# Performance work log

Measured on AMD Instinct MI355X. Metric: run time of the kernel, lower is better.

The kernel has to match this reference:

```python
import jax, jax.numpy as jnp
import numpy as np

NUM_CLASSES = 10
PGD_NUMS = 10
ALPHA = 0.15
# Hardcoded in the original module: sign vector for 10 classes
SIGN_VEC = jnp.array([-1.0] * 4 + [1.0] * 6, dtype=jnp.float32)


def setup_inputs() -> dict:
    key = jax.random.key(0)
    k1, k2, k3 = jax.random.split(key, 3)
    B = 1048576
    logit = jax.random.normal(k1, (B, NUM_CLASSES), dtype=jnp.float32)
    y = jax.random.randint(k2, (B,), 0, NUM_CLASSES, dtype=jnp.int32)
    label_freq = jax.random.randint(k3, (NUM_CLASSES,), 0, PGD_NUMS, dtype=jnp.int32)
    return {"logit": logit, "y": y, "label_freq": label_freq}


def _compute_adv(logit, y):
    # softmax over classes, then per-class mean of softmax rows (one-hot^T @ p)
    p = jax.nn.softmax(logit, axis=-1)  # [B, C]
    sum_class_logit = jax.ops.segment_sum(p, y, num_segments=NUM_CLASSES)  # [C, C]
    counts = jax.ops.segment_sum(jnp.ones(y.shape[0], dtype=logit.dtype), y,
                                 num_segments=NUM_CLASSES)  # [C]
    counts = jnp.where(counts == 0, jnp.asarray(100.0, logit.dtype), counts)
    mean_class_logit = sum_class_logit / counts[:, None]  # [C, C]
    grad = mean_class_logit - jnp.eye(NUM_CLASSES, dtype=logit.dtype)
    # Faithful to torch: norm over dim=0 (columns), then reshape(-1,1) divides row i
    col_norm = jnp.linalg.norm(grad, axis=0)  # [C]
    grad = grad / col_norm[:, None]
    grad = ALPHA * grad * SIGN_VEC[:, None].astype(logit.dtype)
    return grad[y]  # index_select along dim 0 -> [B, C]


def reference(logit, y, label_freq):
    logit_copy = logit

    def step(l, _):
        l_new = l + _compute_adv(l, y)
        return l_new, l_new

    _, logit_steps = jax.lax.scan(step, logit, None, length=PGD_NUMS)  # [P, B, C]

    # Original: logit_news = sum_i logit_steps[label_freq[i]] * (y == i)
    # Since class masks are disjoint, this is a per-sample gather of step label_freq[y[n]].
    steps_per_sample = label_freq[y]  # [B]
    B = logit.shape[0]
    logit_news = logit_steps[steps_per_sample, jnp.arange(B)]  # [B, C]

    # mean cross-entropy
    log_p = jax.nn.log_softmax(logit_news, axis=-1)
    loss_adv = -jnp.mean(jnp.take_along_axis(log_p, y[:, None].astype(jnp.int32), axis=1))
    return loss_adv, logit_news, logit_copy
```

## Files before the change

### kernel.cpp

```cpp
#include <hip/hip_runtime.h>

#define NC 10
#define PGD 10
#define ALPHA 0.15f
#define NTAB 32

#define WS_COUNTS 0
#define WS_STAB   320
#define WS_DGLOB  32320
#define WS_ZERO_N 32320

__device__ __forceinline__ void table_from_stats(
    const float* __restrict__ S_tab_t,
    const float* __restrict__ counts_tab,
    const float* __restrict__ Dprev,
    float* sh_D, float* sh_tmp, float* sh_cnt, float* sh_cn, int tid)
{
    if (tid < 10) {
        float s = 0.f;
        for (int k = 0; k < NTAB; ++k) s += counts_tab[k * 10 + tid];
        sh_cnt[tid] = (s == 0.f) ? 100.f : s;
    }
    if (tid < 100) {
        float s = 0.f;
        for (int k = 0; k < NTAB; ++k) s += S_tab_t[k * 100 + tid];
        sh_tmp[tid] = s;
    }
    __syncthreads();
    if (tid < 100) {
        int c = tid / 10, j = tid - c * 10;
        float g = sh_tmp[tid] / sh_cnt[c] - ((c == j) ? 1.f : 0.f);
        sh_tmp[tid] = g;
    }
    __syncthreads();
    if (tid < 10) {
        float s = 0.f;
        for (int cc = 0; cc < 10; ++cc) { float g = sh_tmp[cc * 10 + tid]; s += g * g; }
        sh_cn[tid] = sqrtf(s);
    }
    __syncthreads();
    if (tid < 100) {
        int c = tid / 10;
        float sign = (c < 4) ? -1.f : 1.f;
        float g = sh_tmp[tid] / sh_cn[c] * (ALPHA * sign);
        sh_D[tid] = (Dprev ? Dprev[tid] : 0.f) + g;
    }
    __syncthreads();
}

__global__ void k_init(float* __restrict__ ws, float* __restrict__ out) {
    int i = blockIdx.x * blockDim.x + threadIdx.x;
    if (i == 0) out[0] = 0.f;
    int gs = gridDim.x * blockDim.x;
    for (int k = i; k < WS_ZERO_N; k += gs) ws[k] = 0.f;
}

__global__ __launch_bounds__(256) void k_step(
    const float* __restrict__ logit, const int* __restrict__ y,
    float* __restrict__ ws, int B, int t , int spt)
{
    __shared__ float sh_D[100];
    __shared__ float sh_tmp[100];
    __shared__ float sh_cnt[10];
    __shared__ float sh_cn[10];
    __shared__ float wtab[4][100];
    __shared__ float ctab[4][10];
    const int tid = threadIdx.x;

    float* counts_tab = ws + WS_COUNTS;
    float* S_tab      = ws + WS_STAB;
    float* D_glob     = ws + WS_DGLOB;

    if (t >= 2) {
        const float* Dprev = (t == 2) ? nullptr : (D_glob + (size_t)(t - 3) * 100);
        table_from_stats(S_tab + (size_t)(t - 2) * (NTAB * 100), counts_tab, Dprev,
                         sh_D, sh_tmp, sh_cnt, sh_cn, tid);
        if (blockIdx.x == 0 && tid < 100) D_glob[(size_t)(t - 2) * 100 + tid] = sh_D[tid];
    }
    for (int i = tid; i < 400; i += 256) (&wtab[0][0])[i] = 0.f;
    if (t == 1) for (int i = tid; i < 40; i += 256) (&ctab[0][0])[i] = 0.f;
    __syncthreads();

    const int w = tid >> 6;
    const int gthreads = gridDim.x * blockDim.x;
    const int base = blockIdx.x * blockDim.x + tid;
    for (int k = 0; k < spt; ++k) {
        int idx = base + k * gthreads;
        if (idx >= B) break;
        int c = y[idx];
        const float2* rp = reinterpret_cast<const float2*>(logit + (size_t)idx * 10);
        float tv[10];
        #pragma unroll
        for (int q = 0; q < 5; ++q) {
            float2 v = rp[q];
            tv[2 * q] = v.x; tv[2 * q + 1] = v.y;
        }
        if (t >= 2) {
            #pragma unroll
            for (int j = 0; j < 10; ++j) tv[j] += sh_D[c * 10 + j];
        }
        float m = tv[0];
        #pragma unroll
        for (int j = 1; j < 10; ++j) m = fmaxf(m, tv[j]);
        float e[10]; float s = 0.f;
        #pragma unroll
        for (int j = 0; j < 10; ++j) { e[j] = __expf(tv[j] - m); s += e[j]; }
        float r = 1.f / s;
        #pragma unroll
        for (int j = 0; j < 10; ++j) unsafeAtomicAdd(&wtab[w][c * 10 + j], e[j] * r);
        if (t == 1) unsafeAtomicAdd(&ctab[w][c], 1.f);
    }
    __syncthreads();

    const int tb = blockIdx.x & (NTAB - 1);
    for (int i = tid; i < 100; i += 256) {
        float s4 = wtab[0][i] + wtab[1][i] + wtab[2][i] + wtab[3][i];
        unsafeAtomicAdd(&S_tab[(size_t)(t - 1) * (NTAB * 100) + tb * 100 + i], s4);
    }
    if (t == 1) {
        for (int i = tid; i < 10; i += 256) {
            float s4 = ctab[0][i] + ctab[1][i] + ctab[2][i] + ctab[3][i];
            unsafeAtomicAdd(&counts_tab[tb * 10 + i], s4);
        }
    }
}

__global__ __launch_bounds__(256) void k_final(
    const float* __restrict__ logit, const int* __restrict__ y,
    const int* __restrict__ label_freq,
    float* __restrict__ out, float* __restrict__ ws, int B, int spt)
{
    __shared__ float sh_D[100];
    __shared__ float sh_tmp[100];
    __shared__ float sh_cnt[10];
    __shared__ float sh_cn[10];
    __shared__ float Dall[PGD][100];
    __shared__ int lf[10];
    __shared__ float wsum[4];
    const int tid = threadIdx.x;

    float* counts_tab = ws + WS_COUNTS;
    float* S_tab      = ws + WS_STAB;
    float* D_glob     = ws + WS_DGLOB;

    table_from_stats(S_tab + (size_t)9 * (NTAB * 100), counts_tab, D_glob + 8 * 100,
                     sh_D, sh_tmp, sh_cnt, sh_cn, tid);
    if (tid < 100) Dall[9][tid] = sh_D[tid];
    for (int i = tid; i < 900; i += 256) Dall[i / 100][i % 100] = D_glob[i];
    if (tid < 10) lf[tid] = label_freq[tid];
    __syncthreads();

    float* news_out = out + 1;
    float* copy_out = out + 1 + (size_t)B * 10;
    const int gthreads = gridDim.x * blockDim.x;
    const int base = blockIdx.x * blockDim.x + tid;
    float acc = 0.f;
    for (int k = 0; k < spt; ++k) {
        int idx = base + k * gthreads;
        if (idx >= B) break;
        int c = y[idx];
        int sel = lf[c];
        const float2* rp = reinterpret_cast<const float2*>(logit + (size_t)idx * 10);
        float xv[10];
        #pragma unroll
        for (int q = 0; q < 5; ++q) {
            float2 v = rp[q];
            xv[2 * q] = v.x; xv[2 * q + 1] = v.y;
        }
        float nv[10];
        #pragma unroll
        for (int j = 0; j < 10; ++j) nv[j] = xv[j] + Dall[sel][c * 10 + j];
        float2* np = reinterpret_cast<float2*>(news_out + (size_t)idx * 10);
        float2* cp = reinterpret_cast<float2*>(copy_out + (size_t)idx * 10);
        #pragma unroll
        for (int q = 0; q < 5; ++q) {
            np[q] = make_float2(nv[2 * q], nv[2 * q + 1]);
            cp[q] = make_float2(xv[2 * q], xv[2 * q + 1]);
        }
        float m = nv[0];
        #pragma unroll
        for (int j = 1; j < 10; ++j) m = fmaxf(m, nv[j]);
        float s = 0.f;
        #pragma unroll
        for (int j = 0; j < 10; ++j) s += __expf(nv[j] - m);
        float lse = __logf(s) + m;
        acc += lse - nv[c];
    }
    #pragma unroll
    for (int off = 32; off > 0; off >>= 1) acc += __shfl_down(acc, off);
    if ((tid & 63) == 0) wsum[tid >> 6] = acc;
    __syncthreads();
    if (tid == 0) {
        float b = wsum[0] + wsum[1] + wsum[2] + wsum[3];
        unsafeAtomicAdd(out, b / (float)B);
    }
}

extern "C" void kernel_launch(void* const* d_in, const int* in_sizes, int n_in,
                              void* d_out, int out_size, void* d_ws, size_t ws_size,
                              hipStream_t stream) {
    const float* logit = (const float*)d_in[0];
    const int* y       = (const int*)d_in[1];
    const int* lf      = (const int*)d_in[2];
    float* out = (float*)d_out;
    float* ws  = (float*)d_ws;
    const int B = in_sizes[0] / 10;

    const int spt = 4;
    const int threads = 256;
    int totalThreads = (B + spt - 1) / spt;
    int blocks = (totalThreads + threads - 1) / threads;

    hipLaunchKernelGGL(k_init, dim3(64), dim3(256), 0, stream, ws, out);
    for (int t = 1; t <= PGD; ++t)
        hipLaunchKernelGGL(k_step, dim3(blocks), dim3(threads), 0, stream,
                           logit, y, ws, B, t, spt);
    hipLaunchKernelGGL(k_final, dim3(blocks), dim3(threads), 0, stream,
                       logit, y, lf, out, ws, B, spt);
}
```

Measured before the change: 624.9 us.

## Prefetch rows before table reduction and spread shared-memory atomics across 32 lane copies

Each thread now issues all of its row and label loads up front, so the memory traffic overlaps the serial per-block reduction of the previous step's statistics into the adjustment table. The per-wave shared-memory accumulation table, which had 4 copies, is replaced by 32 lane-indexed copies laid out [100][32]; this cuts LDS atomic contention, and a rotated read sums the copies afterwards. Samples per thread rise from 4 to 8 and launch bounds now request 2 blocks per CU. Keeping 80 floats per thread in registers raises register pressure, and the larger shared table may lower occupancy.

```diff
diff --git a/kernel.cpp b/kernel.cpp
--- a/kernel.cpp
+++ b/kernel.cpp
@@ -1,52 +1,15 @@
 #include <hip/hip_runtime.h>
 
-#define NC 10
-#define PGD 10
+#define PGD   10
 #define ALPHA 0.15f
-#define NTAB 32
+#define NTAB  32
+#define SPT   8
+#define NTHR  256
 
 #define WS_COUNTS 0
 #define WS_STAB   320
 #define WS_DGLOB  32320
-#define WS_ZERO_N 32320
-
-__device__ __forceinline__ void table_from_stats(
-    const float* __restrict__ S_tab_t,
-    const float* __restrict__ counts_tab,
-    const float* __restrict__ Dprev,
-    float* sh_D, float* sh_tmp, float* sh_cnt, float* sh_cn, int tid)
-{
-    if (tid < 10) {
-        float s = 0.f;
-        for (int k = 0; k < NTAB; ++k) s += counts_tab[k * 10 + tid];
-        sh_cnt[tid] = (s == 0.f) ? 100.f : s;
-    }
-    if (tid < 100) {
-        float s = 0.f;
-        for (int k = 0; k < NTAB; ++k) s += S_tab_t[k * 100 + tid];
-        sh_tmp[tid] = s;
-    }
-    __syncthreads();
-    if (tid < 100) {
-        int c = tid / 10, j = tid - c * 10;
-        float g = sh_tmp[tid] / sh_cnt[c] - ((c == j) ? 1.f : 0.f);
-        sh_tmp[tid] = g;
-    }
-    __syncthreads();
-    if (tid < 10) {
-        float s = 0.f;
-        for (int cc = 0; cc < 10; ++cc) { float g = sh_tmp[cc * 10 + tid]; s += g * g; }
-        sh_cn[tid] = sqrtf(s);
-    }
-    __syncthreads();
-    if (tid < 100) {
-        int c = tid / 10;
-        float sign = (c < 4) ? -1.f : 1.f;
-        float g = sh_tmp[tid] / sh_cn[c] * (ALPHA * sign);
-        sh_D[tid] = (Dprev ? Dprev[tid] : 0.f) + g;
-    }
-    __syncthreads();
-}
+#define WS_ZERO_N 33320
 
 __global__ void k_init(float* __restrict__ ws, float* __restrict__ out) {
     int i = blockIdx.x * blockDim.x + threadIdx.x;
@@ -55,46 +18,93 @@
     for (int k = i; k < WS_ZERO_N; k += gs) ws[k] = 0.f;
 }
 
-__global__ __launch_bounds__(256) void k_step(
+__global__ __launch_bounds__(NTHR, 2) void k_step(
     const float* __restrict__ logit, const int* __restrict__ y,
-    float* __restrict__ ws, int B, int t , int spt)
+    float* __restrict__ ws, int B, int t )
 {
+    __shared__ float tab[100][NTAB];
+    __shared__ float ctab[10][NTAB];
     __shared__ float sh_D[100];
-    __shared__ float sh_tmp[100];
-    __shared__ float sh_cnt[10];
-    __shared__ float sh_cn[10];
-    __shared__ float wtab[4][100];
-    __shared__ float ctab[4][10];
+    __shared__ float shT[100];
+    __shared__ float shCnt[10];
+    __shared__ float shCn[10];
+
     const int tid = threadIdx.x;
+    const int gth = gridDim.x * NTHR;
+    const int base = blockIdx.x * NTHR + tid;
 
     float* counts_tab = ws + WS_COUNTS;
     float* S_tab      = ws + WS_STAB;
     float* D_glob     = ws + WS_DGLOB;
 
+    float xv[SPT][10];
+    int   yc[SPT];
+    #pragma unroll
+    for (int k = 0; k < SPT; ++k) {
+        int idx = base + k * gth;
+        if (idx < B) {
+            yc[k] = y[idx];
+            const float2* rp = reinterpret_cast<const float2*>(logit + (size_t)idx * 10);
+            #pragma unroll
+            for (int q = 0; q < 5; ++q) {
+                float2 v = rp[q];
+                xv[k][2 * q] = v.x; xv[k][2 * q + 1] = v.y;
+            }
+        } else {
+            yc[k] = -1;
+            #pragma unroll
+            for (int j = 0; j < 10; ++j) xv[k][j] = 0.f;
+        }
+    }
+
+    for (int i = tid; i < 100 * NTAB; i += NTHR) (&tab[0][0])[i] = 0.f;
+    if (t == 1) for (int i = tid; i < 10 * NTAB; i += NTHR) (&ctab[0][0])[i] = 0.f;
+
     if (t >= 2) {
-        const float* Dprev = (t == 2) ? nullptr : (D_glob + (size_t)(t - 3) * 100);
-        table_from_stats(S_tab + (size_t)(t - 2) * (NTAB * 100), counts_tab, Dprev,
-                         sh_D, sh_tmp, sh_cnt, sh_cn, tid);
+        const float* Sg = S_tab + (size_t)(t - 2) * (NTAB * 100);
+        if (tid < 10) {
+            float s = 0.f;
+            #pragma unroll
+            for (int k = 0; k < NTAB; ++k) s += counts_tab[k * 10 + tid];
+            shCnt[tid] = (s == 0.f) ? 100.f : s;
+        }
+        if (tid < 100) {
+            float s = 0.f;
+            #pragma unroll
+            for (int k = 0; k < NTAB; ++k) s += Sg[k * 100 + tid];
+            shT[tid] = s;
+        }
+        __syncthreads();
+        if (tid < 100) {
+            int c = tid / 10, j = tid - c * 10;
+            shT[tid] = shT[tid] / shCnt[c] - ((c == j) ? 1.f : 0.f);
+        }
+        __syncthreads();
+        if (tid < 10) {
+            float s = 0.f;
+            for (int cc = 0; cc < 10; ++cc) { float g = shT[cc * 10 + tid]; s += g * g; }
+            shCn[tid] = sqrtf(s);
+        }
+        __syncthreads();
+        if (tid < 100) {
+            int c = tid / 10;
+            float sign = (c < 4) ? -1.f : 1.f;
+            float g = shT[tid] / shCn[c] * (ALPHA * sign);
+            sh_D[tid] = ((t >= 3) ? D_glob[(size_t)(t - 3) * 100 + tid] : 0.f) + g;
+        }
+        __syncthreads();
         if (blockIdx.x == 0 && tid < 100) D_glob[(size_t)(t - 2) * 100 + tid] = sh_D[tid];
     }
-    for (int i = tid; i < 400; i += 256) (&wtab[0][0])[i] = 0.f;
-    if (t == 1) for (int i = tid; i < 40; i += 256) (&ctab[0][0])[i] = 0.f;
     __syncthreads();
 
-    const int w = tid >> 6;
-    const int gthreads = gridDim.x * blockDim.x;
-    const int base = blockIdx.x * blockDim.x + tid;
-    for (int k = 0; k < spt; ++k) {
-        int idx = base + k * gthreads;
-        if (idx >= B) break;
-        int c = y[idx];
-        const float2* rp = reinterpret_cast<const float2*>(logit + (size_t)idx * 10);
+    const int lane31 = tid & 31;
+    #pragma unroll
+    for (int k = 0; k < SPT; ++k) {
+        int c = yc[k];
+        if (c < 0) continue;
         float tv[10];
         #pragma unroll
-        for (int q = 0; q < 5; ++q) {
-            float2 v = rp[q];
-            tv[2 * q] = v.x; tv[2 * q + 1] = v.y;
-        }
+        for (int j = 0; j < 10; ++j) tv[j] = xv[k][j];
         if (t >= 2) {
             #pragma unroll
             for (int j = 0; j < 10; ++j) tv[j] += sh_D[c * 10 + j];
@@ -102,80 +112,126 @@
         float m = tv[0];
         #pragma unroll
         for (int j = 1; j < 10; ++j) m = fmaxf(m, tv[j]);
-        float e[10]; float s = 0.f;
-        #pragma unroll
-        for (int j = 0; j < 10; ++j) { e[j] = __expf(tv[j] - m); s += e[j]; }
+        float s = 0.f;
+        #pragma unroll
+        for (int j = 0; j < 10; ++j) { tv[j] = __expf(tv[j] - m); s += tv[j]; }
         float r = 1.f / s;
         #pragma unroll
-        for (int j = 0; j < 10; ++j) unsafeAtomicAdd(&wtab[w][c * 10 + j], e[j] * r);
-        if (t == 1) unsafeAtomicAdd(&ctab[w][c], 1.f);
+        for (int j = 0; j < 10; ++j) unsafeAtomicAdd(&tab[c * 10 + j][lane31], tv[j] * r);
+        if (t == 1) unsafeAtomicAdd(&ctab[c][lane31], 1.f);
     }
     __syncthreads();
 
     const int tb = blockIdx.x & (NTAB - 1);
-    for (int i = tid; i < 100; i += 256) {
-        float s4 = wtab[0][i] + wtab[1][i] + wtab[2][i] + wtab[3][i];
-        unsafeAtomicAdd(&S_tab[(size_t)(t - 1) * (NTAB * 100) + tb * 100 + i], s4);
-    }
-    if (t == 1) {
-        for (int i = tid; i < 10; i += 256) {
-            float s4 = ctab[0][i] + ctab[1][i] + ctab[2][i] + ctab[3][i];
-            unsafeAtomicAdd(&counts_tab[tb * 10 + i], s4);
-        }
-    }
-}
-
-__global__ __launch_bounds__(256) void k_final(
+    if (tid < 100) {
+        float s = 0.f;
+        #pragma unroll
+        for (int k = 0; k < NTAB; ++k) s += tab[tid][(tid + k) & (NTAB - 1)];
+        unsafeAtomicAdd(&S_tab[(size_t)(t - 1) * (NTAB * 100) + (size_t)tb * 100 + tid], s);
+    }
+    if (t == 1 && tid < 10) {
+        float s = 0.f;
+        #pragma unroll
+        for (int k = 0; k < NTAB; ++k) s += ctab[tid][(tid + k) & (NTAB - 1)];
+        unsafeAtomicAdd(&counts_tab[tb * 10 + tid], s);
+    }
+}
+
+__global__ __launch_bounds__(NTHR, 2) void k_final(
     const float* __restrict__ logit, const int* __restrict__ y,
     const int* __restrict__ label_freq,
-    float* __restrict__ out, float* __restrict__ ws, int B, int spt)
+    float* __restrict__ out, float* __restrict__ ws, int B)
 {
-    __shared__ float sh_D[100];
-    __shared__ float sh_tmp[100];
-    __shared__ float sh_cnt[10];
-    __shared__ float sh_cn[10];
     __shared__ float Dall[PGD][100];
-    __shared__ int lf[10];
+    __shared__ float shT[100];
+    __shared__ float shCnt[10];
+    __shared__ float shCn[10];
+    __shared__ int   lf[10];
     __shared__ float wsum[4];
+
     const int tid = threadIdx.x;
+    const int gth = gridDim.x * NTHR;
+    const int base = blockIdx.x * NTHR + tid;
 
     float* counts_tab = ws + WS_COUNTS;
     float* S_tab      = ws + WS_STAB;
     float* D_glob     = ws + WS_DGLOB;
 
-    table_from_stats(S_tab + (size_t)9 * (NTAB * 100), counts_tab, D_glob + 8 * 100,
-                     sh_D, sh_tmp, sh_cnt, sh_cn, tid);
-    if (tid < 100) Dall[9][tid] = sh_D[tid];
-    for (int i = tid; i < 900; i += 256) Dall[i / 100][i % 100] = D_glob[i];
-    if (tid < 10) lf[tid] = label_freq[tid];
-    __syncthreads();
+    float xv[SPT][10];
+    int   yc[SPT];
+    #pragma unroll
+    for (int k = 0; k < SPT; ++k) {
+        int idx = base + k * gth;
+        if (idx < B) {
+            yc[k] = y[idx];
+            const float2* rp = reinterpret_cast<const float2*>(logit + (size_t)idx * 10);
+            #pragma unroll
+            for (int q = 0; q < 5; ++q) {
+                float2 v = rp[q];
+                xv[k][2 * q] = v.x; xv[k][2 * q + 1] = v.y;
+            }
+        } else {
+            yc[k] = -1;
+            #pragma unroll
+            for (int j = 0; j < 10; ++j) xv[k][j] = 0.f;
+        }
+    }
+
+    {
+        const float* Sg = S_tab + (size_t)9 * (NTAB * 100);
+        if (tid < 10) {
+            float s = 0.f;
+            #pragma unroll
+            for (int k = 0; k < NTAB; ++k) s += counts_tab[k * 10 + tid];
+            shCnt[tid] = (s == 0.f) ? 100.f : s;
+        }
+        if (tid < 100) {
+            float s = 0.f;
+            #pragma unroll
+            for (int k = 0; k < NTAB; ++k) s += Sg[k * 100 + tid];
+            shT[tid] = s;
+        }
+        __syncthreads();
+        if (tid < 100) {
+            int c = tid / 10, j = tid - c * 10;
+            shT[tid] = shT[tid] / shCnt[c] - ((c == j) ? 1.f : 0.f);
+        }
+        __syncthreads();
+        if (tid < 10) {
+            float s = 0.f;
+            for (int cc = 0; cc < 10; ++cc) { float g = shT[cc * 10 + tid]; s += g * g; }
+            shCn[tid] = sqrtf(s);
+        }
+        __syncthreads();
+        if (tid < 100) {
+            int c = tid / 10;
+            float sign = (c < 4) ? -1.f : 1.f;
+            float g = shT[tid] / shCn[c] * (ALPHA * sign);
+            Dall[9][tid] = D_glob[8 * 100 + tid] + g;
+        }
+        for (int i = tid; i < 900; i += NTHR) Dall[i / 100][i % 100] = D_glob[i];
+        if (tid < 10) lf[tid] = label_freq[tid];
+        __syncthreads();
+    }
 
     float* news_out = out + 1;
     float* copy_out = out + 1 + (size_t)B * 10;
-    const int gthreads = gridDim.x * blockDim.x;
-    const int base = blockIdx.x * blockDim.x + tid;
     float acc = 0.f;
-    for (int k = 0; k < spt; ++k) {
-        int idx = base + k * gthreads;
-        if (idx >= B) break;
-        int c = y[idx];
+    #pragma unroll
+    for (int k = 0; k < SPT; ++k) {
+        int idx = base + k * gth;
+        if (idx >= B) continue;
+        int c = yc[k];
         int sel = lf[c];
-        const float2* rp = reinterpret_cast<const float2*>(logit + (size_t)idx * 10);
-        float xv[10];
-        #pragma unroll
-        for (int q = 0; q < 5; ++q) {
-            float2 v = rp[q];
-            xv[2 * q] = v.x; xv[2 * q + 1] = v.y;
-        }
         float nv[10];
         #pragma unroll
-        for (int j = 0; j < 10; ++j) nv[j] = xv[j] + Dall[sel][c * 10 + j];
+        for (int j = 0; j < 10; ++j) nv[j] = xv[k][j] + Dall[sel][c * 10 + j];
         float2* np = reinterpret_cast<float2*>(news_out + (size_t)idx * 10);
         float2* cp = reinterpret_cast<float2*>(copy_out + (size_t)idx * 10);
         #pragma unroll
         for (int q = 0; q < 5; ++q) {
             np[q] = make_float2(nv[2 * q], nv[2 * q + 1]);
-            cp[q] = make_float2(xv[2 * q], xv[2 * q + 1]);
+            cp[q] = make_float2(xv[k][2 * q], xv[k][2 * q + 1]);
         }
         float m = nv[0];
         #pragma unroll
@@ -183,38 +239,32 @@
         float s = 0.f;
         #pragma unroll
         for (int j = 0; j < 10; ++j) s += __expf(nv[j] - m);
-        float lse = __logf(s) + m;
-        acc += lse - nv[c];
+        acc += __logf(s) + m - nv[c];
     }
     #pragma unroll
     for (int off = 32; off > 0; off >>= 1) acc += __shfl_down(acc, off);
     if ((tid & 63) == 0) wsum[tid >> 6] = acc;
     __syncthreads();
-    if (tid == 0) {
-        float b = wsum[0] + wsum[1] + wsum[2] + wsum[3];
-        unsafeAtomicAdd(out, b / (float)B);
-    }
+    if (tid == 0)
+        unsafeAtomicAdd(out, (wsum[0] + wsum[1] + wsum[2] + wsum[3]) / (float)B);
 }
 
 extern "C" void kernel_launch(void* const* d_in, const int* in_sizes, int n_in,
                               void* d_out, int out_size, void* d_ws, size_t ws_size,
                               hipStream_t stream) {
     const float* logit = (const float*)d_in[0];
-    const int* y       = (const int*)d_in[1];
-    const int* lf      = (const int*)d_in[2];
+    const int*   yy    = (const int*)d_in[1];
+    const int*   lf    = (const int*)d_in[2];
     float* out = (float*)d_out;
     float* ws  = (float*)d_ws;
-    const int B = in_sizes[0] / 10;
-
-    const int spt = 4;
-    const int threads = 256;
-    int totalThreads = (B + spt - 1) / spt;
-    int blocks = (totalThreads + threads - 1) / threads;
-
-    hipLaunchKernelGGL(k_init, dim3(64), dim3(256), 0, stream, ws, out);
+    int B = in_sizes[0] / 10;
+
+    int blocks = (B + NTHR * SPT - 1) / (NTHR * SPT);
+
+    hipLaunchKernelGGL(k_init, dim3(64), dim3(NTHR), 0, stream, ws, out);
     for (int t = 1; t <= PGD; ++t)
-        hipLaunchKernelGGL(k_step, dim3(blocks), dim3(threads), 0, stream,
-                           logit, y, ws, B, t, spt);
-    hipLaunchKernelGGL(k_final, dim3(blocks), dim3(threads), 0, stream,
-                       logit, y, lf, out, ws, B, spt);
-}
+        hipLaunchKernelGGL(k_step, dim3(blocks), dim3(NTHR), 0, stream,
+                           logit, yy, ws, B, t);
+    hipLaunchKernelGGL(k_final, dim3(blocks), dim3(NTHR), 0, stream,
+                       logit, yy, lf, out, ws, B);
+}
```

New measurement: 672.2 us. 7.6% more time.
